# Kernel optimization log

Measured on AMD Instinct MI355X. Metric: run time of the kernel, lower is better.

Reference implementation:

```python
import jax, jax.numpy as jnp
import numpy as np

B, D_IN, D, N, C = 512, 512, 256, 500000, 1000
K = 7
TEMP = 0.07
EPS = 1e-12


def setup_inputs() -> dict:
    key = jax.random.key(0)
    ks = jax.random.split(key, 8)
    x = jax.random.normal(ks[0], (B, D_IN), dtype=jnp.float32)
    mean1 = jax.random.normal(ks[1], (D_IN,), dtype=jnp.float32) * 0.1
    std1 = jax.random.uniform(ks[2], (D_IN,), dtype=jnp.float32) + 0.5  # avoid tiny std
    P = jax.random.normal(ks[3], (D_IN, D), dtype=jnp.float32) / np.sqrt(D_IN).astype(np.float32)
    mean2 = jax.random.normal(ks[4], (D,), dtype=jnp.float32) * 0.1
    std2 = jax.random.uniform(ks[5], (D,), dtype=jnp.float32) + 0.5
    train_feats = jax.random.normal(ks[6], (N, D), dtype=jnp.float32)
    train_labels = jax.random.randint(ks[7], (N,), 0, C, dtype=jnp.int32)
    return {"x": x, "mean1": mean1, "std1": std1, "P": P,
            "mean2": mean2, "std2": std2,
            "train_feats": train_feats, "train_labels": train_labels}


def reference(x, mean1, std1, P, mean2, std2, train_feats, train_labels):
    # Preprocessor: standardize -> PCA -> standardize
    z = (x - mean1) / std1          # [B, D_in]
    z = z @ P                        # [B, D]
    z = (z - mean2) / std2
    # L2 normalize (F.normalize with eps clamp)
    norm = jnp.sqrt(jnp.sum(z * z, axis=1, keepdims=True))
    z = z / jnp.maximum(norm, EPS)
    # cosine similarities against the whole train set
    sims = z @ train_feats.T         # [B, N] -- dominant memory traffic
    vals, idx = jax.lax.top_k(sims, K)   # sorted descending, so vals[:, :1] is the max
    lbl = train_labels[idx]              # [B, K]
    w = jnp.exp((vals - vals[:, :1]) / max(TEMP, 1e-6))
    rows = jnp.arange(z.shape[0])[:, None]
    out = jnp.zeros((z.shape[0], C), dtype=jnp.float32).at[rows, lbl].add(w)
    return out
```

## Files before the change

kernel.cpp:

```cpp
#include <hip/hip_runtime.h>

#define N_TRAIN 500000
#define D_FEAT  256
#define B_ROWS  512
#define N_CLS   1000
#define K_TOP   7
#define TAU     3.5f
#define CAP     384
#define CHUNK   512
#define N_CHUNKS 977
#define TR      32
#define DEPTH   4
#define WCAP    64

typedef __attribute__((ext_vector_type(8))) short short8;
typedef __attribute__((ext_vector_type(16))) float f32x16;
typedef const __attribute__((address_space(1))) unsigned int gu32;
typedef __attribute__((address_space(3))) unsigned int lu32;

__device__ __forceinline__ unsigned short f32_to_bf16_rne(float f) {
  unsigned u = __float_as_uint(f);
  u += 0x7FFFu + ((u >> 16) & 1u);
  return (unsigned short)(u >> 16);
}

#if defined(__has_builtin) && __has_builtin(__builtin_amdgcn_perm)
#define PK2(a, b) __builtin_amdgcn_perm(__float_as_uint(b), __float_as_uint(a), 0x07060302u)
#else
#define PK2(a, b) ((__float_as_uint(a) >> 16) | (__float_as_uint(b) & 0xFFFF0000u))
#endif

__global__ __launch_bounds__(256) void prep_kernel(
    const float* __restrict__ x, const float* __restrict__ mean1,
    const float* __restrict__ std1, const float* __restrict__ P,
    const float* __restrict__ mean2, const float* __restrict__ std2,
    float* __restrict__ zf, unsigned short* __restrict__ zb,
    int* __restrict__ cnt) {
  const int b = blockIdx.x;
  const int t = threadIdx.x;
  __shared__ float xn[512 * 5];
  __shared__ float nrm[4];

  if (b == 0) { cnt[t] = 0; cnt[t + 256] = 0; }

  const int r0 = b * 4;
#pragma unroll
  for (int i = 0; i < 8; i++) {
    int f = i * 256 + t;
    int r = f >> 9;
    int k = f & 511;
    float v = x[(r0 + r) * 512 + k];
    xn[k * 5 + r] = (v - mean1[k]) / std1[k];
  }
  __syncthreads();

  float a0 = 0.f, a1 = 0.f, a2 = 0.f, a3 = 0.f;
  const int c = t;
  for (int k = 0; k < 512; k++) {
    float p = P[k * 256 + c];
    a0 = fmaf(xn[k * 5 + 0], p, a0);
    a1 = fmaf(xn[k * 5 + 1], p, a1);
    a2 = fmaf(xn[k * 5 + 2], p, a2);
    a3 = fmaf(xn[k * 5 + 3], p, a3);
  }
  float m2 = mean2[c], s2 = std2[c];
  a0 = (a0 - m2) / s2; a1 = (a1 - m2) / s2;
  a2 = (a2 - m2) / s2; a3 = (a3 - m2) / s2;

  __syncthreads();
  float* zbuf = xn;
  zbuf[0 * 256 + c] = a0; zbuf[1 * 256 + c] = a1;
  zbuf[2 * 256 + c] = a2; zbuf[3 * 256 + c] = a3;
  __syncthreads();

  int wv = t >> 6, lane = t & 63;
  float s = 0.f;
#pragma unroll
  for (int j = 0; j < 4; j++) {
    float v = zbuf[wv * 256 + j * 64 + lane];
    s = fmaf(v, v, s);
  }
#pragma unroll
  for (int off = 32; off; off >>= 1) s += __shfl_down(s, off);
  if (lane == 0) nrm[wv] = sqrtf(s);
  __syncthreads();

  float za[4] = {a0, a1, a2, a3};
#pragma unroll
  for (int r = 0; r < 4; r++) {
    float z = za[r] / fmaxf(nrm[r], 1e-12f);
    zf[(r0 + r) * 256 + c] = z;
    zb[(r0 + r) * 256 + c] = f32_to_bf16_rne(z);
  }
}

__global__ __launch_bounds__(512, 2) void gemm_kernel(
    const unsigned short* __restrict__ zb, const float* __restrict__ T,
    int* __restrict__ cnt, int* __restrict__ cand) {
  const int c_base = blockIdx.x * CHUNK;
  const int n_hi = min(CHUNK, N_TRAIN - c_base);
  const int nt = n_hi >> 5;
  const int tid = threadIdx.x;
  const int w = tid >> 6;
  const int lane = tid & 63;
  const int half = lane >> 5;
  const int l31 = lane & 31;

  __shared__ __align__(1024) char Bsh[DEPTH * TR * 1024];
  __shared__ int wcnt[8];
  __shared__ int wstack[8 * WCAP];

  if (lane == 0) wcnt[w] = 0;

  short8 afr[2][16];
#pragma unroll
  for (int m = 0; m < 2; m++) {
    const char* ab = (const char*)zb + (w * 64 + m * 32 + l31) * 512 + half * 16;
#pragma unroll
    for (int ks = 0; ks < 16; ks++) afr[m][ks] = *(const short8*)(ab + ks * 32);
  }

#define STAGE(x)                                                               \
  do {                                                                         \
    char* buf_ = &Bsh[((x) & 3) * (TR * 1024)];                                \
    const float* gt_ = T + (size_t)(c_base + (x) * TR) * 256;                  \
    _Pragma("unroll")                                                          \
    for (int L = 0; L < 4; L++) {                                              \
      const int row_ = L * 8 + w;                                              \
      const float* gs_ = gt_ + row_ * 256 + ((lane ^ w) << 2);                 \
      __builtin_amdgcn_global_load_lds((gu32*)gs_, (lu32*)(buf_ + row_ * 1024),\
                                       16, 0, 0);                              \
    }                                                                          \
  } while (0)

  STAGE(0); STAGE(1); STAGE(2);

  for (int t = 0; t < nt; t++) {
    {
      int keep = nt - 1 - t;
      if (keep > DEPTH - 2) keep = DEPTH - 2;
      if (keep >= 2)      asm volatile("s_waitcnt vmcnt(8)" ::: "memory");
      else if (keep == 1) asm volatile("s_waitcnt vmcnt(4)" ::: "memory");
      else                asm volatile("s_waitcnt vmcnt(0)" ::: "memory");
    }
    __builtin_amdgcn_s_barrier();
    asm volatile("" ::: "memory");

    if (t + DEPTH - 1 < nt) STAGE(t + DEPTH - 1);

    const char* rowb = &Bsh[(t & 3) * (TR * 1024)] + l31 * 1024;
    const int xr = l31 & 7;

    f32x16 a0, a1;
#pragma unroll
    for (int i = 0; i < 16; i++) { a0[i] = 0.f; a1[i] = 0.f; }

#pragma unroll
    for (int ks = 0; ks < 16; ks++) {
      const int p0 = ((ks * 4 + half * 2) ^ xr) << 4;
      float4 v0 = *(const float4*)(rowb + p0);
      float4 v1 = *(const float4*)(rowb + (p0 ^ 16));
      union { uint4 u; short8 s; } U;
      U.u = make_uint4(PK2(v0.x, v0.y), PK2(v0.z, v0.w),
                       PK2(v1.x, v1.y), PK2(v1.z, v1.w));
      a0 = __builtin_amdgcn_mfma_f32_32x32x16_bf16(afr[0][ks], U.s, a0, 0, 0, 0);
      a1 = __builtin_amdgcn_mfma_f32_32x32x16_bf16(afr[1][ks], U.s, a1, 0, 0, 0);
    }

    const int colg = c_base + t * TR + l31;
#pragma unroll
    for (int reg = 0; reg < 16; reg++) {
      const int rloc = (reg & 3) + 8 * (reg >> 2) + 4 * half;
      if (a0[reg] > TAU) {
        int rowg = w * 64 + rloc;
        int p = atomicAdd(&wcnt[w], 1);
        if (p < WCAP) wstack[w * WCAP + p] = (rowg << 19) | colg;
        else { int q = atomicAdd(&cnt[rowg], 1); if (q < CAP) cand[rowg * CAP + q] = colg; }
      }
      if (a1[reg] > TAU) {
        int rowg = w * 64 + 32 + rloc;
        int p = atomicAdd(&wcnt[w], 1);
        if (p < WCAP) wstack[w * WCAP + p] = (rowg << 19) | colg;
        else { int q = atomicAdd(&cnt[rowg], 1); if (q < CAP) cand[rowg * CAP + q] = colg; }
      }
    }
  }
#undef STAGE

  __syncthreads();
  int mc = wcnt[w];
  if (mc > WCAP) mc = WCAP;
  for (int i = lane; i < mc; i += 64) {
    unsigned e = (unsigned)wstack[w * WCAP + i];
    int rowg = (int)(e >> 19);
    int col = (int)(e & 0x7FFFFu);
    int p = atomicAdd(&cnt[rowg], 1);
    if (p < CAP) cand[rowg * CAP + p] = col;
  }
}

__global__ __launch_bounds__(256) void final_kernel(
    const float* __restrict__ zf, const float* __restrict__ T,
    const int* __restrict__ labels, const int* __restrict__ cnt,
    const int* __restrict__ cand, float* __restrict__ out) {
  const int row = blockIdx.x;
  const int tid = threadIdx.x;
  const int wv = tid >> 6, lane = tid & 63;
  __shared__ float sval[CAP];
  __shared__ int sidx[CAP];
  __shared__ float swv[4];
  __shared__ int swi[4];
  __shared__ float topv[K_TOP];
  __shared__ int topi[K_TOP];

#pragma unroll
  for (int i = 0; i < 4; i++) {
    int c2 = i * 256 + tid;
    if (c2 < N_CLS) out[row * N_CLS + c2] = 0.f;
  }

  int m = cnt[row];
  if (m > CAP) m = CAP;

  for (int i = tid; i < m; i += 256) sidx[i] = cand[row * CAP + i];
  __syncthreads();

  float4 z4 = ((const float4*)(zf + row * 256))[lane];

  for (int i = wv; i < m; i += 4) {
    int col = sidx[i];
    float4 t4 = ((const float4*)(T + (long)col * 256))[lane];
    float s = z4.x * t4.x + z4.y * t4.y + z4.z * t4.z + z4.w * t4.w;
#pragma unroll
    for (int off = 32; off; off >>= 1) s += __shfl_down(s, off);
    if (lane == 0) sval[i] = s;
  }
  __syncthreads();

  for (int t = 0; t < K_TOP; t++) {
    float bv = -1e30f; int bi = -1;
    for (int i = tid; i < m; i += 256) {
      float v = sval[i];
      if (v > bv) { bv = v; bi = i; }
    }
#pragma unroll
    for (int off = 32; off; off >>= 1) {
      float ov = __shfl_down(bv, off);
      int oi = __shfl_down(bi, off);
      if (ov > bv) { bv = ov; bi = oi; }
    }
    if (lane == 0) { swv[wv] = bv; swi[wv] = bi; }
    __syncthreads();
    if (tid == 0) {
      float xv = swv[0]; int xi = swi[0];
      for (int j = 1; j < 4; j++)
        if (swv[j] > xv) { xv = swv[j]; xi = swi[j]; }
      topv[t] = xv; topi[t] = xi;
      if (xi >= 0) sval[xi] = -1e30f;
    }
    __syncthreads();
  }

  if (tid == 0) {
    float v0 = topv[0];
    for (int t = 0; t < K_TOP; t++) {
      if (t < m) {
        int col = sidx[topi[t]];
        float wgt = expf((topv[t] - v0) / 0.07f);
        out[row * N_CLS + labels[col]] += wgt;
      }
    }
  }
}

extern "C" void kernel_launch(void* const* d_in, const int* in_sizes, int n_in,
                              void* d_out, int out_size, void* d_ws, size_t ws_size,
                              hipStream_t stream) {
  const float* x      = (const float*)d_in[0];
  const float* mean1  = (const float*)d_in[1];
  const float* std1   = (const float*)d_in[2];
  const float* P      = (const float*)d_in[3];
  const float* mean2  = (const float*)d_in[4];
  const float* std2   = (const float*)d_in[5];
  const float* T      = (const float*)d_in[6];
  const int*   labels = (const int*)d_in[7];
  float* out = (float*)d_out;

  char* ws = (char*)d_ws;
  float* zf          = (float*)ws;
  unsigned short* zb = (unsigned short*)(ws + 524288);
  int* cnt           = (int*)(ws + 786432);
  int* cand          = (int*)(ws + 788480);

  prep_kernel<<<128, 256, 0, stream>>>(x, mean1, std1, P, mean2, std2, zf, zb, cnt);
  gemm_kernel<<<N_CHUNKS, 512, 0, stream>>>(zb, T, cnt, cand);
  final_kernel<<<B_ROWS, 256, 0, stream>>>(zf, T, labels, cnt, cand, out);
}
```

Baseline: 828.8 us.

## Replace 4-deep async LDS pipeline with register prefetch and bf16 LDS staging

Instead of async global-to-LDS loads of fp32 train features into a 4-stage ring, each tile is now prefetched into registers one step ahead, converted to bf16, and written into a double-buffered LDS area after the MFMA loop. This halves LDS footprint and LDS read traffic, and removes the per-iteration fp32-to-bf16 packing in the inner MFMA loop. The cost is shallower prefetch depth (one tile), which may expose more HBM latency on this memory-bound scan, plus extra register pressure for the prefetch buffers.

```diff
diff --git a/kernel.cpp b/kernel.cpp
--- a/kernel.cpp
+++ b/kernel.cpp
@@ -10,13 +10,10 @@
 #define CHUNK   512
 #define N_CHUNKS 977
 #define TR      32
-#define DEPTH   4
 #define WCAP    64
 
 typedef __attribute__((ext_vector_type(8))) short short8;
 typedef __attribute__((ext_vector_type(16))) float f32x16;
-typedef const __attribute__((address_space(1))) unsigned int gu32;
-typedef __attribute__((address_space(3))) unsigned int lu32;
 
 __device__ __forceinline__ unsigned short f32_to_bf16_rne(float f) {
   unsigned u = __float_as_uint(f);
@@ -106,7 +103,7 @@
   const int half = lane >> 5;
   const int l31 = lane & 31;
 
-  __shared__ __align__(1024) char Bsh[DEPTH * TR * 1024];
+  __shared__ __align__(16) char Bsh[2 * TR * 512];
   __shared__ int wcnt[8];
   __shared__ int wstack[8 * WCAP];
 
@@ -120,51 +117,59 @@
     for (int ks = 0; ks < 16; ks++) afr[m][ks] = *(const short8*)(ab + ks * 32);
   }
 
-#define STAGE(x)                                                               \
-  do {                                                                         \
-    char* buf_ = &Bsh[((x) & 3) * (TR * 1024)];                                \
-    const float* gt_ = T + (size_t)(c_base + (x) * TR) * 256;                  \
-    _Pragma("unroll")                                                          \
-    for (int L = 0; L < 4; L++) {                                              \
-      const int row_ = L * 8 + w;                                              \
-      const float* gs_ = gt_ + row_ * 256 + ((lane ^ w) << 2);                 \
-      __builtin_amdgcn_global_load_lds((gu32*)gs_, (lu32*)(buf_ + row_ * 1024),\
-                                       16, 0, 0);                              \
-    }                                                                          \
-  } while (0)
-
-  STAGE(0); STAGE(1); STAGE(2);
-
-  for (int t = 0; t < nt; t++) {
-    {
-      int keep = nt - 1 - t;
-      if (keep > DEPTH - 2) keep = DEPTH - 2;
-      if (keep >= 2)      asm volatile("s_waitcnt vmcnt(8)" ::: "memory");
-      else if (keep == 1) asm volatile("s_waitcnt vmcnt(4)" ::: "memory");
-      else                asm volatile("s_waitcnt vmcnt(0)" ::: "memory");
-    }
+  const int wb  = (((lane >> 1) ^ w) << 4) | ((lane & 1) << 3);
+  const int rsw = l31 & 7;
+
+  float4 pf[4];
+
+  {
+    const float* g = T + (size_t)c_base * 256 + lane * 4;
+#pragma unroll
+    for (int L = 0; L < 4; L++)
+      pf[L] = *(const float4*)(g + (L * 8 + w) * 256);
+#pragma unroll
+    for (int L = 0; L < 4; L++) {
+      uint2 pk;
+      pk.x = PK2(pf[L].x, pf[L].y);
+      pk.y = PK2(pf[L].z, pf[L].w);
+      *(uint2*)(Bsh + (L * 8 + w) * 512 + wb) = pk;
+    }
+  }
+  asm volatile("s_waitcnt lgkmcnt(0)" ::: "memory");
+
+  for (int t = 0; t < nt; ++t) {
     __builtin_amdgcn_s_barrier();
     asm volatile("" ::: "memory");
 
-    if (t + DEPTH - 1 < nt) STAGE(t + DEPTH - 1);
-
-    const char* rowb = &Bsh[(t & 3) * (TR * 1024)] + l31 * 1024;
-    const int xr = l31 & 7;
-
+    if (t + 1 < nt) {
+      const float* g = T + (size_t)(c_base + (t + 1) * TR) * 256 + lane * 4;
+#pragma unroll
+      for (int L = 0; L < 4; L++)
+        pf[L] = *(const float4*)(g + (L * 8 + w) * 256);
+    }
+
+    const char* rb = Bsh + (t & 1) * (TR * 512) + l31 * 512;
     f32x16 a0, a1;
 #pragma unroll
     for (int i = 0; i < 16; i++) { a0[i] = 0.f; a1[i] = 0.f; }
-
 #pragma unroll
     for (int ks = 0; ks < 16; ks++) {
-      const int p0 = ((ks * 4 + half * 2) ^ xr) << 4;
-      float4 v0 = *(const float4*)(rowb + p0);
-      float4 v1 = *(const float4*)(rowb + (p0 ^ 16));
-      union { uint4 u; short8 s; } U;
-      U.u = make_uint4(PK2(v0.x, v0.y), PK2(v0.z, v0.w),
-                       PK2(v1.x, v1.y), PK2(v1.z, v1.w));
-      a0 = __builtin_amdgcn_mfma_f32_32x32x16_bf16(afr[0][ks], U.s, a0, 0, 0, 0);
-      a1 = __builtin_amdgcn_mfma_f32_32x32x16_bf16(afr[1][ks], U.s, a1, 0, 0, 0);
+      short8 bfr = *(const short8*)(rb + ((((ks << 1) | half) ^ rsw) << 4));
+      a0 = __builtin_amdgcn_mfma_f32_32x32x16_bf16(afr[0][ks], bfr, a0, 0, 0, 0);
+      a1 = __builtin_amdgcn_mfma_f32_32x32x16_bf16(afr[1][ks], bfr, a1, 0, 0, 0);
+    }
+
+    __builtin_amdgcn_sched_barrier(0);
+
+    if (t + 1 < nt) {
+      char* bw = Bsh + ((t + 1) & 1) * (TR * 512);
+#pragma unroll
+      for (int L = 0; L < 4; L++) {
+        uint2 pk;
+        pk.x = PK2(pf[L].x, pf[L].y);
+        pk.y = PK2(pf[L].z, pf[L].w);
+        *(uint2*)(bw + (L * 8 + w) * 512 + wb) = pk;
+      }
     }
 
     const int colg = c_base + t * TR + l31;
@@ -184,16 +189,17 @@
         else { int q = atomicAdd(&cnt[rowg], 1); if (q < CAP) cand[rowg * CAP + q] = colg; }
       }
     }
-  }
-#undef STAGE
+
+    asm volatile("s_waitcnt lgkmcnt(0)" ::: "memory");
+  }
 
   __syncthreads();
   int mc = wcnt[w];
   if (mc > WCAP) mc = WCAP;
   for (int i = lane; i < mc; i += 64) {
-    unsigned e = (unsigned)wstack[w * WCAP + i];
-    int rowg = (int)(e >> 19);
-    int col = (int)(e & 0x7FFFFu);
+    unsigned ev = (unsigned)wstack[w * WCAP + i];
+    int rowg = (int)(ev >> 19);
+    int col = (int)(ev & 0x7FFFFu);
     int p = atomicAdd(&cnt[rowg], 1);
     if (p < CAP) cand[rowg * CAP + p] = col;
   }
```

Result: faster. 784.8 us (-5.3%).
